# Performance work log

Measured on AMD Instinct MI355X. Metric: run time of the kernel, lower is better.

The kernel has to match this reference:

```python
import jax, jax.numpy as jnp
import numpy as np

N_NODES = 100000  # static segment count for segment_sum
DEGREE = 2        # polynomial degree of the Laplacian filter


def setup_inputs() -> dict:
    key = jax.random.key(0)
    k1, k2, k3, k4 = jax.random.split(key, 4)
    N, E, C = N_NODES, 1600000, 32
    x = jax.random.normal(k1, (N, C), dtype=jnp.float32)
    weights = jax.random.normal(k2, (1 + DEGREE,), dtype=jnp.float32)
    edge_src = jax.random.randint(k3, (E,), 0, N, dtype=jnp.int32)
    edge_dst = jax.random.randint(k4, (E,), 0, N, dtype=jnp.int32)
    return {"x": x, "weights": weights, "edge_src": edge_src, "edge_dst": edge_dst}


def reference(x, weights, edge_src, edge_dst):
    """y = (w0 * I + w1 * L + ... + w_d * L^d) @ x with L = D - A,
    computed by the recurrence t_k = L @ t_{k-1} (never materializing L^k)."""
    N = N_NODES
    # node degrees: D[i] = number of edges landing on i
    deg = jax.ops.segment_sum(jnp.ones_like(edge_src, dtype=x.dtype), edge_dst,
                              num_segments=N)  # [N]

    def lap_matvec(t):
        # (L @ t)[i] = deg[i] * t[i] - sum_{(s->i) in E} t[s]
        agg = jax.ops.segment_sum(t[edge_src], edge_dst, num_segments=N)  # [N, C]
        return deg[:, None] * t - agg

    y = weights[0] * x
    t = x
    for k in range(1, 1 + DEGREE):  # fixed small loop over polynomial order
        t = lap_matvec(t)
        y = y + weights[k] * t
    return y
```

## Files before the change

kernel.cpp:

```cpp
#include <hip/hip_runtime.h>

#define C 32
#define BSH 7
#define BNODE 128
#define CAPC 2816
#define NTB 512
#define SRCMASK 0x1FFFF

typedef float f32x4 __attribute__((ext_vector_type(4)));
typedef float f32x2 __attribute__((ext_vector_type(2)));

__device__ __forceinline__ unsigned int f2bf(float f) {
    unsigned int u = __float_as_uint(f);
    return (u + 0x7FFFu + ((u >> 16) & 1u)) >> 16;
}
__device__ __forceinline__ float bflo(unsigned int u) { return __uint_as_float(u << 16); }
__device__ __forceinline__ float bfhi(unsigned int u) { return __uint_as_float(u & 0xFFFF0000u); }

__global__ __launch_bounds__(1024) void phaseA_cvt(const int* __restrict__ src,
                                                   const int* __restrict__ dst,
                                                   int* __restrict__ cursor,
                                                   int* __restrict__ pk,
                                                   const float* __restrict__ x,
                                                   unsigned int* __restrict__ xbh,
                                                   int N, int E, int nbuck, int chunk) {
    extern __shared__ int l[];
    int* lcnt = l;
    int* lcur = l + nbuck;
    int tid = threadIdx.x;
    for (int i = tid; i < nbuck; i += 1024) lcnt[i] = 0;
    __syncthreads();
    int base = blockIdx.x * chunk;
    int end  = min(base + chunk, E);
    for (int e = base + tid; e < end; e += 1024)
        atomicAdd(&lcnt[dst[e] >> BSH], 1);
    __syncthreads();
    for (int i = tid; i < nbuck; i += 1024) {
        int c = lcnt[i];
        lcur[i] = i * CAPC + (c ? atomicAdd(&cursor[i], c) : 0);
    }
    __syncthreads();
    for (int e = base + tid; e < end; e += 1024) {
        int d = dst[e];
        int b = d >> BSH;
        int pos = atomicAdd(&lcur[b], 1);
        pk[pos] = src[e] | ((d & (BNODE - 1)) << 17);
    }
    int total = N * 8;
    int gid = blockIdx.x * 1024 + tid;
    int gth = gridDim.x * 1024;
    for (int i = gid; i < total; i += gth) {
        f32x4 v = *(const f32x4*)(x + (size_t)i * 4);
        uint2 r;
        r.x = f2bf(v.x) | (f2bf(v.y) << 16);
        r.y = f2bf(v.z) | (f2bf(v.w) << 16);
        int node = i >> 3;
        int q = i & 7;
        int half = q >> 2;
        ((uint2*)xbh)[((size_t)half * N + node) * 4 + (q & 3)] = r;
    }
}

__device__ __forceinline__ void accum_h(const unsigned int* __restrict__ tab,
                                        const int* idx, int lo, int hi, int lq,
                                        float& a0, float& a1) {
#define ACC2(u) { a0 += bflo(u); a1 += bfhi(u); }
    int j = lo;
    for (; j + 7 < hi; j += 8) {
        int s0 = idx[j],     s1 = idx[j + 1], s2 = idx[j + 2], s3 = idx[j + 3];
        int s4 = idx[j + 4], s5 = idx[j + 5], s6 = idx[j + 6], s7 = idx[j + 7];
        unsigned int u0 = tab[(size_t)s0 * 8 + lq];
        unsigned int u1 = tab[(size_t)s1 * 8 + lq];
        unsigned int u2 = tab[(size_t)s2 * 8 + lq];
        unsigned int u3 = tab[(size_t)s3 * 8 + lq];
        unsigned int u4 = tab[(size_t)s4 * 8 + lq];
        unsigned int u5 = tab[(size_t)s5 * 8 + lq];
        unsigned int u6 = tab[(size_t)s6 * 8 + lq];
        unsigned int u7 = tab[(size_t)s7 * 8 + lq];
        ACC2(u0) ACC2(u1) ACC2(u2) ACC2(u3) ACC2(u4) ACC2(u5) ACC2(u6) ACC2(u7)
    }
    for (; j + 3 < hi; j += 4) {
        int s0 = idx[j], s1 = idx[j + 1], s2 = idx[j + 2], s3 = idx[j + 3];
        unsigned int u0 = tab[(size_t)s0 * 8 + lq];
        unsigned int u1 = tab[(size_t)s1 * 8 + lq];
        unsigned int u2 = tab[(size_t)s2 * 8 + lq];
        unsigned int u3 = tab[(size_t)s3 * 8 + lq];
        ACC2(u0) ACC2(u1) ACC2(u2) ACC2(u3)
    }
    for (; j < hi; ++j) {
        unsigned int u0 = tab[(size_t)idx[j] * 8 + lq];
        ACC2(u0)
    }
#undef ACC2
}

__global__ __launch_bounds__(NTB) void phaseB_mv1(int* __restrict__ pk,
                                                  const int* __restrict__ cursor,
                                                  int* __restrict__ row_start,
                                                  int* __restrict__ ideg,
                                                  const unsigned int* __restrict__ xbh,
                                                  unsigned int* __restrict__ t1h, int N) {
    __shared__ int ent[CAPC];
    __shared__ int sorted[CAPC];
    __shared__ int h[BNODE];
    __shared__ int ss[BNODE];
    __shared__ int cur[BNODE];
    int b = blockIdx.x;
    int tid = threadIdx.x;
    int n0 = b << BSH;
    int base = b * CAPC;
    int cnt = min(cursor[b], CAPC);

    if (tid < BNODE) h[tid] = 0;
    __syncthreads();
    for (int i = tid; i < cnt; i += NTB) {
        int en = __builtin_nontemporal_load(&pk[base + i]);
        ent[i] = en;
        atomicAdd(&h[en >> 17], 1);
    }
    __syncthreads();
    int v = 0;
    if (tid < BNODE) { v = h[tid]; ss[tid] = v; }
    __syncthreads();
    for (int off = 1; off < BNODE; off <<= 1) {
        int u = 0;
        if (tid < BNODE && tid >= off) u = ss[tid - off];
        __syncthreads();
        if (tid < BNODE) ss[tid] += u;
        __syncthreads();
    }
    if (tid < BNODE) {
        int exc = ss[tid] - v;
        int n = n0 + tid;
        if (n < N) { row_start[n] = base + exc; ideg[n] = v; }
        cur[tid] = exc;
    }
    __syncthreads();
    for (int i = tid; i < cnt; i += NTB) {
        int en = ent[i];
        int pos = atomicAdd(&cur[en >> 17], 1);
        sorted[pos] = en & SRCMASK;
    }
    __syncthreads();
    for (int i = tid; i < cnt; i += NTB)
        pk[base + i] = sorted[i];

    for (int hf = 0; hf < 2; ++hf) {
        const unsigned int* tab = xbh + (size_t)hf * N * 8;
        unsigned int* ttab = t1h + (size_t)hf * N * 8;
        for (int it = tid; it < BNODE * 8; it += NTB) {
            int r = it >> 3;
            int lq = it & 7;
            int n = n0 + r;
            if (n >= N) continue;
            int hi = ss[r];
            int lo = hi - h[r];
            float a0 = 0.f, a1 = 0.f;
            accum_h(tab, sorted, lo, hi, lq, a0, a1);
            unsigned int xs = tab[(size_t)n * 8 + lq];
            float fdg = (float)h[r];
            unsigned int rr = f2bf(fdg * bflo(xs) - a0)
                            | (f2bf(fdg * bfhi(xs) - a1) << 16);
            ttab[(size_t)n * 8 + lq] = rr;
        }
    }
}

__global__ __launch_bounds__(NTB) void gather2_lds(const unsigned int* __restrict__ xbh,
        const unsigned int* __restrict__ t1h, const int* __restrict__ pk,
        const int* __restrict__ cursor, const int* __restrict__ row_start,
        const int* __restrict__ ideg, const float* __restrict__ wts,
        float* __restrict__ y, int N) {
    __shared__ int stg[CAPC];
    int b = blockIdx.x;
    int tid = threadIdx.x;
    int n0 = b << BSH;
    int base = b * CAPC;
    int cnt = min(cursor[b], CAPC);
    for (int i = tid; i < cnt; i += NTB)
        stg[i] = __builtin_nontemporal_load(&pk[base + i]);
    __syncthreads();
    float w0 = wts[0], w1 = wts[1], w2 = wts[2];
    for (int hf = 0; hf < 2; ++hf) {
        const unsigned int* xtab = xbh + (size_t)hf * N * 8;
        const unsigned int* ttab = t1h + (size_t)hf * N * 8;
        for (int it = tid; it < BNODE * 8; it += NTB) {
            int r = it >> 3;
            int lq = it & 7;
            int n = n0 + r;
            if (n >= N) continue;
            int dg = ideg[n];
            int lo = row_start[n] - base;
            int hi = lo + dg;
            float a0 = 0.f, a1 = 0.f;
            accum_h(ttab, stg, lo, hi, lq, a0, a1);
            unsigned int xs = xtab[(size_t)n * 8 + lq];
            unsigned int ts = ttab[(size_t)n * 8 + lq];
            float fdg = (float)dg;
            f32x2 yv;
            yv.x = w0 * bflo(xs) + w1 * bflo(ts) + w2 * (fdg * bflo(ts) - a0);
            yv.y = w0 * bfhi(xs) + w1 * bfhi(ts) + w2 * (fdg * bfhi(ts) - a1);
            __builtin_nontemporal_store(yv,
                (f32x2*)(y + (size_t)n * C + hf * 16 + lq * 2));
        }
    }
}

extern "C" void kernel_launch(void* const* d_in, const int* in_sizes, int n_in,
                              void* d_out, int out_size, void* d_ws, size_t ws_size,
                              hipStream_t stream) {
    const float* x    = (const float*)d_in[0];
    const float* wts  = (const float*)d_in[1];
    const int*   esrc = (const int*)d_in[2];
    const int*   edst = (const int*)d_in[3];
    float*       y    = (float*)d_out;

    const int N = in_sizes[0] / C;
    const int E = in_sizes[2];
    const int nbuck = (N + BNODE - 1) >> BSH;
    const int nc = N * C;

    char* p = (char*)d_ws;
    auto align16 = [](size_t s) { return (s + 15) & ~(size_t)15; };
    int* cursor    = (int*)p; p += align16((size_t)nbuck * 4);
    int* row_start = (int*)p; p += align16((size_t)N * 4);
    int* ideg      = (int*)p; p += align16((size_t)N * 4);
    int* pk        = (int*)p; p += align16((size_t)nbuck * CAPC * 4);
    unsigned int* xbh = (unsigned int*)p; p += align16((size_t)nc * 2);
    unsigned int* t1h = (unsigned int*)p; p += align16((size_t)nc * 2);
    (void)ws_size;

    (void)hipMemsetAsync(cursor, 0, (size_t)nbuck * 4, stream);

    const int ABLK = 512;
    const int chunk = (E + ABLK - 1) / ABLK;
    const size_t lds_a = (size_t)nbuck * 2 * 4;

    phaseA_cvt<<<ABLK, 1024, lds_a, stream>>>(esrc, edst, cursor, pk, x, xbh,
                                              N, E, nbuck, chunk);
    phaseB_mv1<<<nbuck, NTB, 0, stream>>>(pk, cursor, row_start, ideg,
                                          xbh, t1h, N);
    gather2_lds<<<nbuck, NTB, 0, stream>>>(xbh, t1h, pk, cursor, row_start,
                                           ideg, wts, y, N);
}
```

Baseline: 161.4 us.

## Switch bf16 feature tables to row-major layout with 16-byte gathers

Drops the split-half layout of the bf16 node tables. Each node's 32 channels are now stored contiguously (64 bytes), and each thread gathers a 16-byte vector covering 8 channels per neighbour instead of 4 bytes covering 2 channels. Four threads per node replace eight threads per half over two passes, so each neighbour row is fetched as one full 64-byte segment and index reads from LDS drop. In exchange there are fewer threads per block of work and more accumulator registers per thread, which may reduce latency hiding on the random gathers.

```diff
diff --git a/kernel.cpp b/kernel.cpp
--- a/kernel.cpp
+++ b/kernel.cpp
@@ -8,7 +8,7 @@
 #define SRCMASK 0x1FFFF
 
 typedef float f32x4 __attribute__((ext_vector_type(4)));
-typedef float f32x2 __attribute__((ext_vector_type(2)));
+typedef unsigned int u32x4 __attribute__((ext_vector_type(4)));
 
 __device__ __forceinline__ unsigned int f2bf(float f) {
     unsigned int u = __float_as_uint(f);
@@ -22,7 +22,7 @@
                                                    int* __restrict__ cursor,
                                                    int* __restrict__ pk,
                                                    const float* __restrict__ x,
-                                                   unsigned int* __restrict__ xbh,
+                                                   uint2* __restrict__ xb2,
                                                    int N, int E, int nbuck, int chunk) {
     extern __shared__ int l[];
     int* lcnt = l;
@@ -54,52 +54,51 @@
         uint2 r;
         r.x = f2bf(v.x) | (f2bf(v.y) << 16);
         r.y = f2bf(v.z) | (f2bf(v.w) << 16);
-        int node = i >> 3;
-        int q = i & 7;
-        int half = q >> 2;
-        ((uint2*)xbh)[((size_t)half * N + node) * 4 + (q & 3)] = r;
-    }
-}
-
-__device__ __forceinline__ void accum_h(const unsigned int* __restrict__ tab,
-                                        const int* idx, int lo, int hi, int lq,
-                                        float& a0, float& a1) {
-#define ACC2(u) { a0 += bflo(u); a1 += bfhi(u); }
+        xb2[i] = r;
+    }
+}
+
+__device__ __forceinline__ void accum_q(const u32x4* __restrict__ tab,
+                                        const int* idx, int lo, int hi, int lqq,
+                                        float& a0, float& a1, float& a2, float& a3,
+                                        float& a4, float& a5, float& a6, float& a7) {
+#define ACC8(u) { a0 += bflo(u.x); a1 += bfhi(u.x); a2 += bflo(u.y); a3 += bfhi(u.y); \
+                  a4 += bflo(u.z); a5 += bfhi(u.z); a6 += bflo(u.w); a7 += bfhi(u.w); }
     int j = lo;
     for (; j + 7 < hi; j += 8) {
         int s0 = idx[j],     s1 = idx[j + 1], s2 = idx[j + 2], s3 = idx[j + 3];
         int s4 = idx[j + 4], s5 = idx[j + 5], s6 = idx[j + 6], s7 = idx[j + 7];
-        unsigned int u0 = tab[(size_t)s0 * 8 + lq];
-        unsigned int u1 = tab[(size_t)s1 * 8 + lq];
-        unsigned int u2 = tab[(size_t)s2 * 8 + lq];
-        unsigned int u3 = tab[(size_t)s3 * 8 + lq];
-        unsigned int u4 = tab[(size_t)s4 * 8 + lq];
-        unsigned int u5 = tab[(size_t)s5 * 8 + lq];
-        unsigned int u6 = tab[(size_t)s6 * 8 + lq];
-        unsigned int u7 = tab[(size_t)s7 * 8 + lq];
-        ACC2(u0) ACC2(u1) ACC2(u2) ACC2(u3) ACC2(u4) ACC2(u5) ACC2(u6) ACC2(u7)
+        u32x4 u0 = tab[(size_t)s0 * 4 + lqq];
+        u32x4 u1 = tab[(size_t)s1 * 4 + lqq];
+        u32x4 u2 = tab[(size_t)s2 * 4 + lqq];
+        u32x4 u3 = tab[(size_t)s3 * 4 + lqq];
+        u32x4 u4 = tab[(size_t)s4 * 4 + lqq];
+        u32x4 u5 = tab[(size_t)s5 * 4 + lqq];
+        u32x4 u6 = tab[(size_t)s6 * 4 + lqq];
+        u32x4 u7 = tab[(size_t)s7 * 4 + lqq];
+        ACC8(u0) ACC8(u1) ACC8(u2) ACC8(u3) ACC8(u4) ACC8(u5) ACC8(u6) ACC8(u7)
     }
     for (; j + 3 < hi; j += 4) {
         int s0 = idx[j], s1 = idx[j + 1], s2 = idx[j + 2], s3 = idx[j + 3];
-        unsigned int u0 = tab[(size_t)s0 * 8 + lq];
-        unsigned int u1 = tab[(size_t)s1 * 8 + lq];
-        unsigned int u2 = tab[(size_t)s2 * 8 + lq];
-        unsigned int u3 = tab[(size_t)s3 * 8 + lq];
-        ACC2(u0) ACC2(u1) ACC2(u2) ACC2(u3)
+        u32x4 u0 = tab[(size_t)s0 * 4 + lqq];
+        u32x4 u1 = tab[(size_t)s1 * 4 + lqq];
+        u32x4 u2 = tab[(size_t)s2 * 4 + lqq];
+        u32x4 u3 = tab[(size_t)s3 * 4 + lqq];
+        ACC8(u0) ACC8(u1) ACC8(u2) ACC8(u3)
     }
     for (; j < hi; ++j) {
-        unsigned int u0 = tab[(size_t)idx[j] * 8 + lq];
-        ACC2(u0)
-    }
-#undef ACC2
+        u32x4 u0 = tab[(size_t)idx[j] * 4 + lqq];
+        ACC8(u0)
+    }
+#undef ACC8
 }
 
 __global__ __launch_bounds__(NTB) void phaseB_mv1(int* __restrict__ pk,
                                                   const int* __restrict__ cursor,
                                                   int* __restrict__ row_start,
                                                   int* __restrict__ ideg,
-                                                  const unsigned int* __restrict__ xbh,
-                                                  unsigned int* __restrict__ t1h, int N) {
+                                                  const u32x4* __restrict__ xb4,
+                                                  u32x4* __restrict__ t14, int N) {
     __shared__ int ent[CAPC];
     __shared__ int sorted[CAPC];
     __shared__ int h[BNODE];
@@ -145,29 +144,29 @@
     for (int i = tid; i < cnt; i += NTB)
         pk[base + i] = sorted[i];
 
-    for (int hf = 0; hf < 2; ++hf) {
-        const unsigned int* tab = xbh + (size_t)hf * N * 8;
-        unsigned int* ttab = t1h + (size_t)hf * N * 8;
-        for (int it = tid; it < BNODE * 8; it += NTB) {
-            int r = it >> 3;
-            int lq = it & 7;
-            int n = n0 + r;
-            if (n >= N) continue;
-            int hi = ss[r];
-            int lo = hi - h[r];
-            float a0 = 0.f, a1 = 0.f;
-            accum_h(tab, sorted, lo, hi, lq, a0, a1);
-            unsigned int xs = tab[(size_t)n * 8 + lq];
-            float fdg = (float)h[r];
-            unsigned int rr = f2bf(fdg * bflo(xs) - a0)
-                            | (f2bf(fdg * bfhi(xs) - a1) << 16);
-            ttab[(size_t)n * 8 + lq] = rr;
-        }
-    }
-}
-
-__global__ __launch_bounds__(NTB) void gather2_lds(const unsigned int* __restrict__ xbh,
-        const unsigned int* __restrict__ t1h, const int* __restrict__ pk,
+    for (int it = tid; it < BNODE * 4; it += NTB) {
+        int r = it >> 2;
+        int lqq = it & 3;
+        int n = n0 + r;
+        if (n >= N) continue;
+        int hi = ss[r];
+        int lo = hi - h[r];
+        float a0 = 0.f, a1 = 0.f, a2 = 0.f, a3 = 0.f;
+        float a4 = 0.f, a5 = 0.f, a6 = 0.f, a7 = 0.f;
+        accum_q(xb4, sorted, lo, hi, lqq, a0, a1, a2, a3, a4, a5, a6, a7);
+        u32x4 xs = xb4[(size_t)n * 4 + lqq];
+        float fdg = (float)h[r];
+        u32x4 rr;
+        rr.x = f2bf(fdg * bflo(xs.x) - a0) | (f2bf(fdg * bfhi(xs.x) - a1) << 16);
+        rr.y = f2bf(fdg * bflo(xs.y) - a2) | (f2bf(fdg * bfhi(xs.y) - a3) << 16);
+        rr.z = f2bf(fdg * bflo(xs.z) - a4) | (f2bf(fdg * bfhi(xs.z) - a5) << 16);
+        rr.w = f2bf(fdg * bflo(xs.w) - a6) | (f2bf(fdg * bfhi(xs.w) - a7) << 16);
+        t14[(size_t)n * 4 + lqq] = rr;
+    }
+}
+
+__global__ __launch_bounds__(NTB) void gather2_lds(const u32x4* __restrict__ xb4,
+        const u32x4* __restrict__ t14, const int* __restrict__ pk,
         const int* __restrict__ cursor, const int* __restrict__ row_start,
         const int* __restrict__ ideg, const float* __restrict__ wts,
         float* __restrict__ y, int N) {
@@ -181,28 +180,32 @@
         stg[i] = __builtin_nontemporal_load(&pk[base + i]);
     __syncthreads();
     float w0 = wts[0], w1 = wts[1], w2 = wts[2];
-    for (int hf = 0; hf < 2; ++hf) {
-        const unsigned int* xtab = xbh + (size_t)hf * N * 8;
-        const unsigned int* ttab = t1h + (size_t)hf * N * 8;
-        for (int it = tid; it < BNODE * 8; it += NTB) {
-            int r = it >> 3;
-            int lq = it & 7;
-            int n = n0 + r;
-            if (n >= N) continue;
-            int dg = ideg[n];
-            int lo = row_start[n] - base;
-            int hi = lo + dg;
-            float a0 = 0.f, a1 = 0.f;
-            accum_h(ttab, stg, lo, hi, lq, a0, a1);
-            unsigned int xs = xtab[(size_t)n * 8 + lq];
-            unsigned int ts = ttab[(size_t)n * 8 + lq];
-            float fdg = (float)dg;
-            f32x2 yv;
-            yv.x = w0 * bflo(xs) + w1 * bflo(ts) + w2 * (fdg * bflo(ts) - a0);
-            yv.y = w0 * bfhi(xs) + w1 * bfhi(ts) + w2 * (fdg * bfhi(ts) - a1);
-            __builtin_nontemporal_store(yv,
-                (f32x2*)(y + (size_t)n * C + hf * 16 + lq * 2));
-        }
+    for (int it = tid; it < BNODE * 4; it += NTB) {
+        int r = it >> 2;
+        int lqq = it & 3;
+        int n = n0 + r;
+        if (n >= N) continue;
+        int dg = ideg[n];
+        int lo = row_start[n] - base;
+        int hi = lo + dg;
+        float a0 = 0.f, a1 = 0.f, a2 = 0.f, a3 = 0.f;
+        float a4 = 0.f, a5 = 0.f, a6 = 0.f, a7 = 0.f;
+        accum_q(t14, stg, lo, hi, lqq, a0, a1, a2, a3, a4, a5, a6, a7);
+        u32x4 xs = xb4[(size_t)n * 4 + lqq];
+        u32x4 ts = t14[(size_t)n * 4 + lqq];
+        float fdg = (float)dg;
+        f32x4 y0, y1;
+        y0.x = w0 * bflo(xs.x) + w1 * bflo(ts.x) + w2 * (fdg * bflo(ts.x) - a0);
+        y0.y = w0 * bfhi(xs.x) + w1 * bfhi(ts.x) + w2 * (fdg * bfhi(ts.x) - a1);
+        y0.z = w0 * bflo(xs.y) + w1 * bflo(ts.y) + w2 * (fdg * bflo(ts.y) - a2);
+        y0.w = w0 * bfhi(xs.y) + w1 * bfhi(ts.y) + w2 * (fdg * bfhi(ts.y) - a3);
+        y1.x = w0 * bflo(xs.z) + w1 * bflo(ts.z) + w2 * (fdg * bflo(ts.z) - a4);
+        y1.y = w0 * bfhi(xs.z) + w1 * bfhi(ts.z) + w2 * (fdg * bfhi(ts.z) - a5);
+        y1.z = w0 * bflo(xs.w) + w1 * bflo(ts.w) + w2 * (fdg * bflo(ts.w) - a6);
+        y1.w = w0 * bfhi(xs.w) + w1 * bfhi(ts.w) + w2 * (fdg * bfhi(ts.w) - a7);
+        float* yo = y + (size_t)n * C + lqq * 8;
+        __builtin_nontemporal_store(y0, (f32x4*)yo);
+        __builtin_nontemporal_store(y1, (f32x4*)(yo + 4));
     }
 }
 
@@ -226,8 +229,8 @@
     int* row_start = (int*)p; p += align16((size_t)N * 4);
     int* ideg      = (int*)p; p += align16((size_t)N * 4);
     int* pk        = (int*)p; p += align16((size_t)nbuck * CAPC * 4);
-    unsigned int* xbh = (unsigned int*)p; p += align16((size_t)nc * 2);
-    unsigned int* t1h = (unsigned int*)p; p += align16((size_t)nc * 2);
+    u32x4* xb4     = (u32x4*)p; p += align16((size_t)nc * 2);
+    u32x4* t14     = (u32x4*)p; p += align16((size_t)nc * 2);
     (void)ws_size;
 
     (void)hipMemsetAsync(cursor, 0, (size_t)nbuck * 4, stream);
@@ -236,10 +239,10 @@
     const int chunk = (E + ABLK - 1) / ABLK;
     const size_t lds_a = (size_t)nbuck * 2 * 4;
 
-    phaseA_cvt<<<ABLK, 1024, lds_a, stream>>>(esrc, edst, cursor, pk, x, xbh,
-                                              N, E, nbuck, chunk);
+    phaseA_cvt<<<ABLK, 1024, lds_a, stream>>>(esrc, edst, cursor, pk, x,
+                                              (uint2*)xb4, N, E, nbuck, chunk);
     phaseB_mv1<<<nbuck, NTB, 0, stream>>>(pk, cursor, row_start, ideg,
-                                          xbh, t1h, N);
-    gather2_lds<<<nbuck, NTB, 0, stream>>>(xbh, t1h, pk, cursor, row_start,
+                                          xb4, t14, N);
+    gather2_lds<<<nbuck, NTB, 0, stream>>>(xb4, t14, pk, cursor, row_start,
                                            ideg, wts, y, N);
 }
```

Result: faster. 151.7 us (-6.0%).
